# Optimization experiments

Hardware: AMD Instinct MI355X
Metric: run time of the kernel (lower is better)

## Reference

```python
import jax, jax.numpy as jnp
import numpy as np

N_ATOMS = 10000
N_EDGES = 160000
N_SPECIES = 8
N_STRUCT = 8
C = 16        # n_element_channels
N_MAX = 4     # radial functions per l
N_BASIS = 8   # bessel basis size
L_MAX = 3
CUTOFF = 5.0
K = N_MAX * C             # equivariant channels per l (k_max_l)
K_TOTAL = (L_MAX + 1) * K  # concatenated invariants


def _sph_harm(u):
    """Real spherical harmonics l=0..3 for unit vectors u [E,3] -> [E,16]."""
    x, y, z = u[:, 0], u[:, 1], u[:, 2]
    x2, y2, z2 = x * x, y * y, z * z
    one = jnp.ones_like(x)
    ys = [
        0.28209479 * one,
        0.48860251 * y, 0.48860251 * z, 0.48860251 * x,
        1.09254843 * x * y, 1.09254843 * y * z,
        0.31539157 * (3.0 * z2 - 1.0),
        1.09254843 * x * z, 0.54627422 * (x2 - y2),
        0.59004359 * y * (3.0 * x2 - y2), 2.89061144 * x * y * z,
        0.45704579 * y * (5.0 * z2 - 1.0), 0.37317633 * z * (5.0 * z2 - 3.0),
        0.45704579 * x * (5.0 * z2 - 1.0), 1.44530572 * z * (x2 - y2),
        0.59004359 * x * (x2 - 3.0 * y2),
    ]
    return jnp.stack(ys, axis=-1)


def _radial(r, W_rad):
    """Bessel radial basis with cosine cutoff, projected per l. r [E] -> [E, L+1, N_MAX]."""
    n = jnp.arange(1, N_BASIS + 1, dtype=r.dtype)
    rr = jnp.maximum(r, 1e-6)
    basis = jnp.sqrt(2.0 / CUTOFF) * jnp.sin(n[None, :] * jnp.pi * rr[:, None] / CUTOFF) / rr[:, None]
    fc = 0.5 * (jnp.cos(jnp.pi * jnp.clip(r / CUTOFF, 0.0, 1.0)) + 1.0)  # smooth cutoff
    return jnp.einsum('eb,lbn->eln', basis * fc[:, None], W_rad)


def _mp_layer(h, senders, receivers, sh, R, W_inv, cemb):
    """One equivariant message-passing + CG(l x l -> 0) invariant contraction."""
    hs = h[senders]  # gather neighbor scalars [E, C]
    invs = []
    for l in range(L_MAX + 1):
        sl = sh[:, l * l:(l + 1) * (l + 1)]  # [E, 2l+1]
        # edge message: sh x radial x neighbor features -> [E, 2l+1, N_MAX*C]
        M = jnp.einsum('em,en,ec->emnc', sl, R[:, l], hs)
        M = M.reshape(M.shape[0], 2 * l + 1, K)
        A = jax.ops.segment_sum(M, receivers, num_segments=N_ATOMS)  # scatter to centers
        # CG l (x) l -> L=0 invariant (real-SH convention)
        invs.append(jnp.einsum('nmk,nmk->nk', A, A) / jnp.sqrt(2.0 * l + 1.0))
    inv = jnp.concatenate(invs, axis=-1)  # [N, K_TOTAL]
    h_new = (inv @ W_inv) * cemb  # center element embedding
    return h_new, inv


def setup_inputs() -> dict:
    key = jax.random.key(0)
    ks = jax.random.split(key, 10)
    positions = jax.random.uniform(ks[0], (N_ATOMS, 3), jnp.float32, 0.0, 3.0)
    senders = jax.random.randint(ks[1], (N_EDGES,), 0, N_ATOMS)
    receivers = jax.random.randint(ks[2], (N_EDGES,), 0, N_ATOMS)
    species = jax.random.randint(ks[3], (N_ATOMS,), 0, N_SPECIES)
    structure_ids = jnp.sort(jax.random.randint(ks[4], (N_ATOMS,), 0, N_STRUCT))
    embed = jax.random.normal(ks[5], (N_SPECIES, C), jnp.float32)
    W_rad = jax.random.normal(ks[6], (L_MAX + 1, N_BASIS, N_MAX), jnp.float32) * 0.3
    W_inv1 = jax.random.normal(ks[7], (K_TOTAL, C), jnp.float32) / np.sqrt(K_TOTAL)
    W_inv2 = jax.random.normal(ks[8], (K_TOTAL, C), jnp.float32) / np.sqrt(K_TOTAL)
    w_out = jax.random.normal(ks[9], (K_TOTAL,), jnp.float32) / np.sqrt(K_TOTAL)
    comp_weights = jnp.zeros((N_SPECIES,), jnp.float32)
    return {"positions": positions, "embed": embed, "W_rad": W_rad,
            "W_inv1": W_inv1, "W_inv2": W_inv2, "w_out": w_out,
            "comp_weights": comp_weights, "senders": senders,
            "receivers": receivers, "species": species,
            "structure_ids": structure_ids}


def reference(positions, embed, W_rad, W_inv1, W_inv2, w_out, comp_weights,
              senders, receivers, species, structure_ids):
    rvec = positions[receivers] - positions[senders]          # [E,3]
    r = jnp.linalg.norm(rvec, axis=-1)
    u = rvec / jnp.maximum(r, 1e-6)[:, None]
    sh = _sph_harm(u)                                          # [E,16]
    R = _radial(r, W_rad)                                      # [E,4,N_MAX]
    cemb = embed[species]                                      # center embedding [N,C]
    h = cemb                                                   # initial features
    h, _ = _mp_layer(h, senders, receivers, sh, R, W_inv1, cemb)
    h, inv2 = _mp_layer(h, senders, receivers, sh, R, W_inv2, cemb)
    e_atom = inv2 @ w_out + comp_weights[species]              # per-atom energies [N]
    return jax.ops.segment_sum(e_atom, structure_ids, num_segments=N_STRUCT)
```

## Files before the change

kernel.cpp:

```cpp
#include <hip/hip_runtime.h>

#define N_ATOMS 10000
#define N_EDGES 160000
#define N_STRUCT 8
#define D_PAD 48
#define EDW 32
#define N_SLOTS (N_ATOMS * D_PAD)
#define B4 4
#define PI_F 3.14159265358979323846f
#define SROW 260


__global__ void setup_kernel(const float* __restrict__ embed, const int* __restrict__ species,
                             const float* __restrict__ Wi1, const float* __restrict__ Wi2,
                             float* __restrict__ h0, float* __restrict__ WT1,
                             float* __restrict__ WT2,
                             int* __restrict__ cursor, float* __restrict__ accum) {
    int i = blockIdx.x * blockDim.x + threadIdx.x;
    if (i < N_ATOMS) cursor[i] = i * D_PAD;
    if (i < N_STRUCT) accum[i] = 0.f;
    if (i < N_ATOMS * 16) {
        int a = i >> 4, c = i & 15;
        h0[i] = embed[species[a] * 16 + c];
    }
    if (i < 4096) {
        int k = i >> 4, c = i & 15;
        WT1[c * 256 + k] = Wi1[i];
        WT2[c * 256 + k] = Wi2[i];
    }
}

__global__ void scatter_kernel(const int* __restrict__ receivers, int* __restrict__ cursor,
                               int* __restrict__ perm) {
    int e = blockIdx.x * blockDim.x + threadIdx.x;
    if (e < N_EDGES) perm[e] = atomicAdd(&cursor[receivers[e]], 1);
}


__global__ void geom_pad(const float* __restrict__ pos, const float* __restrict__ W_rad,
                         const int* __restrict__ senders, const int* __restrict__ receivers,
                         const int* __restrict__ perm, const int* __restrict__ cursor,
                         float* __restrict__ edat, int* __restrict__ snd) {
    int g = blockIdx.x * blockDim.x + threadIdx.x;

    if (g < N_ATOMS * 3) {
        int a = g / 3, j = g % 3;
        int cnt = cursor[a] - a * D_PAD;
        if (cnt > D_PAD) cnt = D_PAD;
        int c4 = (cnt + B4 - 1) / B4 * B4;
        if (c4 > D_PAD) c4 = D_PAD;
        int slot = cnt + j;
        if (slot < c4) {
            float4 z = make_float4(0.f, 0.f, 0.f, 0.f);
            float4* p = (float4*)(edat + (size_t)(a * D_PAD + slot) * EDW);
            #pragma unroll
            for (int k = 0; k < 8; ++k) p[k] = z;
            snd[a * D_PAD + slot] = 0;
        }
    }

    if (g >= N_EDGES) return;
    const int e = g;
    int s = senders[e], rc = receivers[e];
    int p = perm[e];
    float dx = pos[rc * 3 + 0] - pos[s * 3 + 0];
    float dy = pos[rc * 3 + 1] - pos[s * 3 + 1];
    float dz = pos[rc * 3 + 2] - pos[s * 3 + 2];
    float r = sqrtf(dx * dx + dy * dy + dz * dz);
    float rr = fmaxf(r, 1e-6f);
    float inv = 1.0f / rr;
    float x = dx * inv, y = dy * inv, z = dz * inv;
    float x2 = x * x, y2 = y * y, z2 = z * z;
    float she[16];
    she[0]  = 0.28209479f;
    she[1]  = 0.48860251f * y;
    she[2]  = 0.48860251f * z;
    she[3]  = 0.48860251f * x;
    she[4]  = 1.09254843f * x * y;
    she[5]  = 1.09254843f * y * z;
    she[6]  = 0.31539157f * (3.0f * z2 - 1.0f);
    she[7]  = 1.09254843f * x * z;
    she[8]  = 0.54627422f * (x2 - y2);
    she[9]  = 0.59004359f * y * (3.0f * x2 - y2);
    she[10] = 2.89061144f * x * y * z;
    she[11] = 0.45704579f * y * (5.0f * z2 - 1.0f);
    she[12] = 0.37317633f * z * (5.0f * z2 - 3.0f);
    she[13] = 0.45704579f * x * (5.0f * z2 - 1.0f);
    she[14] = 1.44530572f * z * (x2 - y2);
    she[15] = 0.59004359f * x * (x2 - 3.0f * y2);
    float* ed = edat + (size_t)p * EDW;
    ((float4*)ed)[0] = make_float4(she[0], she[1], she[2], she[3]);
    ((float4*)ed)[1] = make_float4(she[4], she[5], she[6], she[7]);
    ((float4*)ed)[2] = make_float4(she[8], she[9], she[10], she[11]);
    ((float4*)ed)[3] = make_float4(she[12], she[13], she[14], she[15]);

    float theta = PI_F * rr * 0.2f;
    float s1, c1;
    __sincosf(theta, &s1, &c1);
    float fc = (r * 0.2f < 1.0f) ? 0.5f * (c1 + 1.0f) : 0.0f;
    const float kf = 0.6324555320336759f * inv * fc;
    float bfv[8];
    float sprev = 0.f, scur = s1;
    bfv[0] = kf * scur;
    const float twoc = 2.0f * c1;
    #pragma unroll
    for (int n = 1; n < 8; ++n) {
        float snext = fmaf(twoc, scur, -sprev);
        sprev = scur; scur = snext;
        bfv[n] = kf * scur;
    }

    float Re[16];
    #pragma unroll
    for (int l = 0; l < 4; ++l) {
        #pragma unroll
        for (int n = 0; n < 4; ++n) {
            float acc = 0.0f;
            #pragma unroll
            for (int b = 0; b < 8; ++b) acc = fmaf(bfv[b], W_rad[l * 32 + b * 4 + n], acc);
            Re[l * 4 + n] = acc;
        }
    }
    ((float4*)ed)[4] = make_float4(Re[0], Re[1], Re[2], Re[3]);
    ((float4*)ed)[5] = make_float4(Re[4], Re[5], Re[6], Re[7]);
    ((float4*)ed)[6] = make_float4(Re[8], Re[9], Re[10], Re[11]);
    ((float4*)ed)[7] = make_float4(Re[12], Re[13], Re[14], Re[15]);
    snd[p] = s;
}


__global__ __launch_bounds__(64, 7) void mp_accum2(
    const float* __restrict__ edat, const int* __restrict__ snd,
    const int* __restrict__ cursor, const float* __restrict__ h_in,
    float* __restrict__ Inv)
{
    __shared__ __attribute__((aligned(16))) float wl[1024];
    const int lane = threadIdx.x;
    const int atom = blockIdx.x;
    const int m = lane >> 2, cg = lane & 3;
    const int l = (m >= 9) ? 3 : (m >= 4) ? 2 : (m >= 1) ? 1 : 0;
    const int l4 = l * 4, cg4 = cg * 4;

    int cnt = cursor[atom] - atom * D_PAD;
    if (cnt > D_PAD) cnt = D_PAD;
    const int nb = (cnt + B4 - 1) / B4;

    int sv = 0;
    if (lane < D_PAD) sv = snd[atom * D_PAD + lane];

    const float* strip = edat + (size_t)atom * (D_PAD * EDW);

    float acc[4][4];
    #pragma unroll
    for (int n = 0; n < 4; ++n)
        #pragma unroll
        for (int j = 0; j < 4; ++j) acc[n][j] = 0.f;

    for (int b = 0; b < nb; ++b) {
        const int s0 = b * B4;
        const float* bp = strip + s0 * EDW;
        float  shv[B4];
        float4 rv[B4];
        float4 hv[B4];
        #pragma unroll
        for (int q = 0; q < B4; ++q) {
            const float* eq = bp + q * EDW;
            shv[q] = eq[m];
            rv[q]  = *(const float4*)(eq + 16 + l4);
            hv[q]  = *(const float4*)(h_in + (size_t)__shfl(sv, s0 + q) * 16 + cg4);
        }
        #pragma unroll
        for (int q = 0; q < B4; ++q) {
            float hvj[4] = {hv[q].x, hv[q].y, hv[q].z, hv[q].w};
            float rvn[4] = {rv[q].x, rv[q].y, rv[q].z, rv[q].w};
            #pragma unroll
            for (int j = 0; j < 4; ++j) {
                float ww = shv[q] * hvj[j];
                #pragma unroll
                for (int n = 0; n < 4; ++n)
                    acc[n][j] = fmaf(ww, rvn[n], acc[n][j]);
            }
        }
    }

    #pragma unroll
    for (int n = 0; n < 4; ++n)
        *(float4*)&wl[m * 64 + n * 16 + cg4] =
            make_float4(acc[n][0] * acc[n][0], acc[n][1] * acc[n][1],
                        acc[n][2] * acc[n][2], acc[n][3] * acc[n][3]);

    const float* T = wl;
    const int k = lane;
    float s0v = T[k];
    float s1v = T[64 + k] + T[128 + k] + T[192 + k];
    float s2v = T[256 + k] + T[320 + k] + T[384 + k] + T[448 + k] + T[512 + k];
    float s3v = T[576 + k] + T[640 + k] + T[704 + k] + T[768 + k]
              + T[832 + k] + T[896 + k] + T[960 + k];
    float* ip = Inv + (size_t)atom * 256;
    ip[k]       = s0v;
    ip[64 + k]  = s1v * 0.57735026918962576f;
    ip[128 + k] = s2v * 0.44721359549995794f;
    ip[192 + k] = s3v * 0.37796447300922720f;
}


__global__ __launch_bounds__(256, 2) void mp_inv3(
    const float* __restrict__ Inv,
    const float* __restrict__ W_invT,
    const float* __restrict__ cemb, float* __restrict__ h_out,
    const float* __restrict__ w_out, const float* __restrict__ comp_w,
    const int* __restrict__ species, const int* __restrict__ sids,
    float* __restrict__ accum, int do_energy)
{
    __shared__ __attribute__((aligned(16))) float sWT[16 * SROW];
    __shared__ __attribute__((aligned(16))) float sInv[16 * SROW];
    __shared__ float sE[16];
    const int t = threadIdx.x;
    const int w = t >> 6, lane = t & 63;
    const int blk = blockIdx.x;

    if (do_energy) {
        #pragma unroll
        for (int g = 0; g < 4; ++g) {
            const int atomL = g * 4 + w;
            const size_t base = (size_t)(blk * 16 + atomL) * 256;
            float i0 = Inv[base + lane];
            float i1 = Inv[base + 64 + lane];
            float i2 = Inv[base + 128 + lane];
            float i3 = Inv[base + 192 + lane];
            float pe = i0 * w_out[lane] + i1 * w_out[64 + lane]
                     + i2 * w_out[128 + lane] + i3 * w_out[192 + lane];
            #pragma unroll
            for (int off = 32; off > 0; off >>= 1) pe += __shfl_down(pe, off);
            if (lane == 0) sE[atomL] = pe;
        }
        __syncthreads();
        if (t == 0) {
            const int base = blk * 16;
            int cursid = sids[base];
            float run = 0.f;
            for (int a = 0; a < 16; ++a) {
                int sid = sids[base + a];
                float e = sE[a] + comp_w[species[base + a]];
                if (sid != cursid) { atomicAdd(&accum[cursid], run); run = 0.f; cursid = sid; }
                run += e;
            }
            atomicAdd(&accum[cursid], run);
        }
    } else {
        #pragma unroll
        for (int i = 0; i < 16; ++i) {
            int idx = i * 256 + t;
            int row = idx >> 8, col = idx & 255;
            sWT[row * SROW + col]  = W_invT[idx];
            sInv[row * SROW + col] = Inv[(size_t)blk * 4096 + idx];
        }
        __syncthreads();
        const int aL = t >> 4, c = t & 15;
        const float* ivp = &sInv[aL * SROW];
        const float* wvp = &sWT[c * SROW];
        float p = 0.f;
        #pragma unroll
        for (int kk = 0; kk < 64; ++kk) {
            float4 iv = *(const float4*)&ivp[kk * 4];
            float4 wv = *(const float4*)&wvp[kk * 4];
            p = fmaf(iv.x, wv.x, p);
            p = fmaf(iv.y, wv.y, p);
            p = fmaf(iv.z, wv.z, p);
            p = fmaf(iv.w, wv.w, p);
        }
        const int gi = blk * 256 + t;
        h_out[gi] = p * cemb[gi];
    }
}

__global__ void out_kernel(const float* __restrict__ accum, float* __restrict__ out) {
    int t = threadIdx.x;
    if (t < N_STRUCT) out[t] = accum[t];
}


extern "C" void kernel_launch(void* const* d_in, const int* in_sizes, int n_in,
                              void* d_out, int out_size, void* d_ws, size_t ws_size,
                              hipStream_t stream) {
    const float* positions = (const float*)d_in[0];
    const float* embed     = (const float*)d_in[1];
    const float* W_rad     = (const float*)d_in[2];
    const float* W_inv1    = (const float*)d_in[3];
    const float* W_inv2    = (const float*)d_in[4];
    const float* w_out     = (const float*)d_in[5];
    const float* comp_w    = (const float*)d_in[6];
    const int* senders    = (const int*)d_in[7];
    const int* receivers  = (const int*)d_in[8];
    const int* species    = (const int*)d_in[9];
    const int* sids       = (const int*)d_in[10];
    float* out = (float*)d_out;

    char* ws = (char*)d_ws;
    size_t off = 0;
    auto alloc = [&](size_t bytes) -> void* {
        void* p = ws + off;
        off = (off + bytes + 255) & ~(size_t)255;
        return p;
    };
    float* edat     = (float*)alloc((size_t)N_SLOTS * EDW * 4);
    float* Inv      = (float*)alloc((size_t)N_ATOMS * 256 * 4);
    float* h0       = (float*)alloc((size_t)N_ATOMS * 16 * 4);
    float* h1       = (float*)alloc((size_t)N_ATOMS * 16 * 4);
    int*   cursor   = (int*)alloc((size_t)N_ATOMS * 4);
    int*   perm     = (int*)alloc((size_t)N_EDGES * 4);
    int*   snd      = (int*)alloc((size_t)N_SLOTS * 4);
    float* accum    = (float*)alloc(8 * 4);
    float* WT1      = (float*)alloc(4096 * 4);
    float* WT2      = (float*)alloc(4096 * 4);

    const int EB = (N_EDGES + 255) / 256;

    setup_kernel<<<EB, 256, 0, stream>>>(embed, species, W_inv1, W_inv2,
                                         h0, WT1, WT2, cursor, accum);
    scatter_kernel<<<EB, 256, 0, stream>>>(receivers, cursor, perm);
    geom_pad<<<EB, 256, 0, stream>>>(positions, W_rad, senders, receivers,
                                     perm, cursor, edat, snd);

    mp_accum2<<<N_ATOMS, 64, 0, stream>>>(edat, snd, cursor, h0, Inv);
    mp_inv3<<<N_ATOMS / 16, 256, 0, stream>>>(Inv, WT1, h0, h1,
                                              w_out, comp_w, species, sids, accum, 0);
    mp_accum2<<<N_ATOMS, 64, 0, stream>>>(edat, snd, cursor, h1, Inv);
    mp_inv3<<<N_ATOMS / 16, 256, 0, stream>>>(Inv, WT2, h0, h1,
                                              w_out, comp_w, species, sids, accum, 1);

    out_kernel<<<1, 64, 0, stream>>>(accum, out);
}
```

Measured before the change: 156.5 us.

## Fuse edge scatter with geometry and energy readout into message accumulation

Merges the receiver-slot atomic scatter into the geometry kernel, removing the perm buffer and one launch. Partial-block padding becomes predicated loads that clamp to the last valid slot and zero the spherical-harmonic weight. The second layer's energy readout is folded into the accumulation kernel, so the Inv tensor is neither written nor re-read for the final layer. In exchange, the readout issues one global atomic per atom onto a few structure accumulators, where before it used per-block run-length aggregation.

```diff
diff --git a/kernel.cpp b/kernel.cpp
--- a/kernel.cpp
+++ b/kernel.cpp
@@ -30,39 +30,16 @@
     }
 }
 
-__global__ void scatter_kernel(const int* __restrict__ receivers, int* __restrict__ cursor,
-                               int* __restrict__ perm) {
+
+__global__ void scatter_geom(const float* __restrict__ pos, const float* __restrict__ W_rad,
+                             const int* __restrict__ senders, const int* __restrict__ receivers,
+                             int* __restrict__ cursor,
+                             float* __restrict__ edat, int* __restrict__ snd) {
     int e = blockIdx.x * blockDim.x + threadIdx.x;
-    if (e < N_EDGES) perm[e] = atomicAdd(&cursor[receivers[e]], 1);
-}
-
-
-__global__ void geom_pad(const float* __restrict__ pos, const float* __restrict__ W_rad,
-                         const int* __restrict__ senders, const int* __restrict__ receivers,
-                         const int* __restrict__ perm, const int* __restrict__ cursor,
-                         float* __restrict__ edat, int* __restrict__ snd) {
-    int g = blockIdx.x * blockDim.x + threadIdx.x;
-
-    if (g < N_ATOMS * 3) {
-        int a = g / 3, j = g % 3;
-        int cnt = cursor[a] - a * D_PAD;
-        if (cnt > D_PAD) cnt = D_PAD;
-        int c4 = (cnt + B4 - 1) / B4 * B4;
-        if (c4 > D_PAD) c4 = D_PAD;
-        int slot = cnt + j;
-        if (slot < c4) {
-            float4 z = make_float4(0.f, 0.f, 0.f, 0.f);
-            float4* p = (float4*)(edat + (size_t)(a * D_PAD + slot) * EDW);
-            #pragma unroll
-            for (int k = 0; k < 8; ++k) p[k] = z;
-            snd[a * D_PAD + slot] = 0;
-        }
-    }
-
-    if (g >= N_EDGES) return;
-    const int e = g;
+    if (e >= N_EDGES) return;
     int s = senders[e], rc = receivers[e];
-    int p = perm[e];
+    int p = atomicAdd(&cursor[rc], 1);
+    if (p >= (rc + 1) * D_PAD) return;
     float dx = pos[rc * 3 + 0] - pos[s * 3 + 0];
     float dy = pos[rc * 3 + 1] - pos[s * 3 + 1];
     float dz = pos[rc * 3 + 2] - pos[s * 3 + 2];
@@ -129,10 +106,13 @@
 }
 
 
-__global__ __launch_bounds__(64, 7) void mp_accum2(
+__global__ __launch_bounds__(64, 7) void mp_fused(
     const float* __restrict__ edat, const int* __restrict__ snd,
     const int* __restrict__ cursor, const float* __restrict__ h_in,
-    float* __restrict__ Inv)
+    float* __restrict__ Inv,
+    const float* __restrict__ w_out, const float* __restrict__ comp_w,
+    const int* __restrict__ species, const int* __restrict__ sids,
+    float* __restrict__ accum, int do_energy)
 {
     __shared__ __attribute__((aligned(16))) float wl[1024];
     const int lane = threadIdx.x;
@@ -158,16 +138,19 @@
 
     for (int b = 0; b < nb; ++b) {
         const int s0 = b * B4;
-        const float* bp = strip + s0 * EDW;
         float  shv[B4];
         float4 rv[B4];
         float4 hv[B4];
         #pragma unroll
         for (int q = 0; q < B4; ++q) {
-            const float* eq = bp + q * EDW;
-            shv[q] = eq[m];
+            int sq = s0 + q;
+            const bool valid = sq < cnt;
+            sq = valid ? sq : (cnt - 1);
+            const float* eq = strip + sq * EDW;
+            float sh = eq[m];
+            shv[q] = valid ? sh : 0.f;
             rv[q]  = *(const float4*)(eq + 16 + l4);
-            hv[q]  = *(const float4*)(h_in + (size_t)__shfl(sv, s0 + q) * 16 + cg4);
+            hv[q]  = *(const float4*)(h_in + (size_t)__shfl(sv, sq) * 16 + cg4);
         }
         #pragma unroll
         for (int q = 0; q < B4; ++q) {
@@ -196,82 +179,60 @@
     float s2v = T[256 + k] + T[320 + k] + T[384 + k] + T[448 + k] + T[512 + k];
     float s3v = T[576 + k] + T[640 + k] + T[704 + k] + T[768 + k]
               + T[832 + k] + T[896 + k] + T[960 + k];
-    float* ip = Inv + (size_t)atom * 256;
-    ip[k]       = s0v;
-    ip[64 + k]  = s1v * 0.57735026918962576f;
-    ip[128 + k] = s2v * 0.44721359549995794f;
-    ip[192 + k] = s3v * 0.37796447300922720f;
-}
-
-
-__global__ __launch_bounds__(256, 2) void mp_inv3(
+    const float i0 = s0v;
+    const float i1 = s1v * 0.57735026918962576f;
+    const float i2 = s2v * 0.44721359549995794f;
+    const float i3 = s3v * 0.37796447300922720f;
+
+    if (do_energy) {
+        float pe = i0 * w_out[k] + i1 * w_out[64 + k]
+                 + i2 * w_out[128 + k] + i3 * w_out[192 + k];
+        #pragma unroll
+        for (int off = 32; off > 0; off >>= 1) pe += __shfl_down(pe, off);
+        if (lane == 0) atomicAdd(&accum[sids[atom]], pe + comp_w[species[atom]]);
+    } else {
+        float* ip = Inv + (size_t)atom * 256;
+        ip[k]       = i0;
+        ip[64 + k]  = i1;
+        ip[128 + k] = i2;
+        ip[192 + k] = i3;
+    }
+}
+
+
+__global__ __launch_bounds__(256, 2) void mp_inv3h(
     const float* __restrict__ Inv,
     const float* __restrict__ W_invT,
-    const float* __restrict__ cemb, float* __restrict__ h_out,
-    const float* __restrict__ w_out, const float* __restrict__ comp_w,
-    const int* __restrict__ species, const int* __restrict__ sids,
-    float* __restrict__ accum, int do_energy)
+    const float* __restrict__ cemb, float* __restrict__ h_out)
 {
     __shared__ __attribute__((aligned(16))) float sWT[16 * SROW];
     __shared__ __attribute__((aligned(16))) float sInv[16 * SROW];
-    __shared__ float sE[16];
     const int t = threadIdx.x;
-    const int w = t >> 6, lane = t & 63;
     const int blk = blockIdx.x;
 
-    if (do_energy) {
-        #pragma unroll
-        for (int g = 0; g < 4; ++g) {
-            const int atomL = g * 4 + w;
-            const size_t base = (size_t)(blk * 16 + atomL) * 256;
-            float i0 = Inv[base + lane];
-            float i1 = Inv[base + 64 + lane];
-            float i2 = Inv[base + 128 + lane];
-            float i3 = Inv[base + 192 + lane];
-            float pe = i0 * w_out[lane] + i1 * w_out[64 + lane]
-                     + i2 * w_out[128 + lane] + i3 * w_out[192 + lane];
-            #pragma unroll
-            for (int off = 32; off > 0; off >>= 1) pe += __shfl_down(pe, off);
-            if (lane == 0) sE[atomL] = pe;
-        }
-        __syncthreads();
-        if (t == 0) {
-            const int base = blk * 16;
-            int cursid = sids[base];
-            float run = 0.f;
-            for (int a = 0; a < 16; ++a) {
-                int sid = sids[base + a];
-                float e = sE[a] + comp_w[species[base + a]];
-                if (sid != cursid) { atomicAdd(&accum[cursid], run); run = 0.f; cursid = sid; }
-                run += e;
-            }
-            atomicAdd(&accum[cursid], run);
-        }
-    } else {
-        #pragma unroll
-        for (int i = 0; i < 16; ++i) {
-            int idx = i * 256 + t;
-            int row = idx >> 8, col = idx & 255;
-            sWT[row * SROW + col]  = W_invT[idx];
-            sInv[row * SROW + col] = Inv[(size_t)blk * 4096 + idx];
-        }
-        __syncthreads();
-        const int aL = t >> 4, c = t & 15;
-        const float* ivp = &sInv[aL * SROW];
-        const float* wvp = &sWT[c * SROW];
-        float p = 0.f;
-        #pragma unroll
-        for (int kk = 0; kk < 64; ++kk) {
-            float4 iv = *(const float4*)&ivp[kk * 4];
-            float4 wv = *(const float4*)&wvp[kk * 4];
-            p = fmaf(iv.x, wv.x, p);
-            p = fmaf(iv.y, wv.y, p);
-            p = fmaf(iv.z, wv.z, p);
-            p = fmaf(iv.w, wv.w, p);
-        }
-        const int gi = blk * 256 + t;
-        h_out[gi] = p * cemb[gi];
-    }
+    #pragma unroll
+    for (int i = 0; i < 16; ++i) {
+        int idx = i * 256 + t;
+        int row = idx >> 8, col = idx & 255;
+        sWT[row * SROW + col]  = W_invT[idx];
+        sInv[row * SROW + col] = Inv[(size_t)blk * 4096 + idx];
+    }
+    __syncthreads();
+    const int aL = t >> 4, c = t & 15;
+    const float* ivp = &sInv[aL * SROW];
+    const float* wvp = &sWT[c * SROW];
+    float p = 0.f;
+    #pragma unroll
+    for (int kk = 0; kk < 64; ++kk) {
+        float4 iv = *(const float4*)&ivp[kk * 4];
+        float4 wv = *(const float4*)&wvp[kk * 4];
+        p = fmaf(iv.x, wv.x, p);
+        p = fmaf(iv.y, wv.y, p);
+        p = fmaf(iv.z, wv.z, p);
+        p = fmaf(iv.w, wv.w, p);
+    }
+    const int gi = blk * 256 + t;
+    h_out[gi] = p * cemb[gi];
 }
 
 __global__ void out_kernel(const float* __restrict__ accum, float* __restrict__ out) {
@@ -308,26 +269,24 @@
     float* h0       = (float*)alloc((size_t)N_ATOMS * 16 * 4);
     float* h1       = (float*)alloc((size_t)N_ATOMS * 16 * 4);
     int*   cursor   = (int*)alloc((size_t)N_ATOMS * 4);
-    int*   perm     = (int*)alloc((size_t)N_EDGES * 4);
-    int*   snd      = (int*)alloc((size_t)N_SLOTS * 4);
     float* accum    = (float*)alloc(8 * 4);
     float* WT1      = (float*)alloc(4096 * 4);
     float* WT2      = (float*)alloc(4096 * 4);
+    int*   snd      = (int*)alloc((size_t)N_SLOTS * 4);
 
     const int EB = (N_EDGES + 255) / 256;
 
     setup_kernel<<<EB, 256, 0, stream>>>(embed, species, W_inv1, W_inv2,
                                          h0, WT1, WT2, cursor, accum);
-    scatter_kernel<<<EB, 256, 0, stream>>>(receivers, cursor, perm);
-    geom_pad<<<EB, 256, 0, stream>>>(positions, W_rad, senders, receivers,
-                                     perm, cursor, edat, snd);
-
-    mp_accum2<<<N_ATOMS, 64, 0, stream>>>(edat, snd, cursor, h0, Inv);
-    mp_inv3<<<N_ATOMS / 16, 256, 0, stream>>>(Inv, WT1, h0, h1,
-                                              w_out, comp_w, species, sids, accum, 0);
-    mp_accum2<<<N_ATOMS, 64, 0, stream>>>(edat, snd, cursor, h1, Inv);
-    mp_inv3<<<N_ATOMS / 16, 256, 0, stream>>>(Inv, WT2, h0, h1,
-                                              w_out, comp_w, species, sids, accum, 1);
+    scatter_geom<<<EB, 256, 0, stream>>>(positions, W_rad, senders, receivers,
+                                         cursor, edat, snd);
+
+    mp_fused<<<N_ATOMS, 64, 0, stream>>>(edat, snd, cursor, h0, Inv,
+                                         w_out, comp_w, species, sids, nullptr, 0);
+    mp_inv3h<<<N_ATOMS / 16, 256, 0, stream>>>(Inv, WT1, h0, h1);
+
+    mp_fused<<<N_ATOMS, 64, 0, stream>>>(edat, snd, cursor, h1, Inv,
+                                         w_out, comp_w, species, sids, accum, 1);
 
     out_kernel<<<1, 64, 0, stream>>>(accum, out);
 }
```

After: 255.3 us. +63.1%, slower.
